# Kernel tuning notes

Measured on AMD Instinct MI355X. Metric: run time of the kernel, lower is better.

Reference implementation:

```python
import jax, jax.numpy as jnp
import numpy as np

N = 50000      # nodes
E = 600000     # edges (avg degree 12)
F_IN = 128     # num_features
H = 128        # hidden_feats (== F_IN so both conv layers share weight shapes)
C = 10         # num_classes
L = 2          # num_layers


def setup_inputs() -> dict:
    key = jax.random.key(0)
    ks = jax.random.split(key, 12)
    s = 0.05
    x = jax.random.normal(ks[0], (N, F_IN), dtype=jnp.float32)
    edge_index = jax.random.randint(ks[1], (2, E), 0, N, dtype=jnp.int64)
    # Stacked per-layer TransformerConv params (heads=1): query/key/value/skip linears.
    Wq = jax.random.normal(ks[2], (L, H, F_IN), dtype=jnp.float32) * s
    bq = jax.random.normal(ks[3], (L, H), dtype=jnp.float32) * s
    Wk = jax.random.normal(ks[4], (L, H, F_IN), dtype=jnp.float32) * s
    bk = jax.random.normal(ks[5], (L, H), dtype=jnp.float32) * s
    Wv = jax.random.normal(ks[6], (L, H, F_IN), dtype=jnp.float32) * s
    bv = jax.random.normal(ks[7], (L, H), dtype=jnp.float32) * s
    Ws = jax.random.normal(ks[8], (L, H, F_IN), dtype=jnp.float32) * s
    bs = jax.random.normal(ks[9], (L, H), dtype=jnp.float32) * s
    fc_W = jax.random.normal(ks[10], (C, H), dtype=jnp.float32) * s
    fc_b = jax.random.normal(ks[11], (C,), dtype=jnp.float32) * s
    return {"x": x, "edge_index": edge_index, "Wq": Wq, "bq": bq, "Wk": Wk,
            "bk": bk, "Wv": Wv, "bv": bv, "Ws": Ws, "bs": bs,
            "fc_W": fc_W, "fc_b": fc_b}


def _transformer_conv(h, src, dst, Wq, bq, Wk, bk, Wv, bv, Ws, bs):
    # PyG TransformerConv, heads=1, concat=True, root_weight=True, eval mode.
    d = Wq.shape[0]
    scale = 1.0 / np.sqrt(d).astype(np.float32)
    q = h @ Wq.T + bq          # [N, d]
    k = h @ Wk.T + bk          # [N, d]
    v = h @ Wv.T + bv          # [N, d]
    # per-edge attention score: <q_dst, k_src> / sqrt(d)
    scores = jnp.sum(q[dst] * k[src], axis=-1) * scale   # [E]
    # scatter-softmax over incoming edges of each destination node
    m = jax.ops.segment_max(scores, dst, num_segments=N)           # [N]
    e = jnp.exp(scores - m[dst])                                   # [E]
    denom = jax.ops.segment_sum(e, dst, num_segments=N)            # [N]
    alpha = e / denom[dst]                                         # [E]
    agg = jax.ops.segment_sum(alpha[:, None] * v[src], dst, num_segments=N)  # [N, d]
    return agg + (h @ Ws.T + bs)  # root/skip connection


def reference(x, edge_index, Wq, bq, Wk, bk, Wv, bv, Ws, bs, fc_W, fc_b):
    src = edge_index[0]
    dst = edge_index[1]
    h = x
    for l in range(L):  # fixed small layer loop
        h = _transformer_conv(h, src, dst, Wq[l], bq[l], Wk[l], bk[l],
                              Wv[l], bv[l], Ws[l], bs[l])
        h = jax.nn.relu(h)  # dropout is identity in eval mode
    logits = h @ fc_W.T + fc_b  # [N, C]
    return jax.nn.log_softmax(logits, axis=1)
```

## Files before the change

kernel.cpp:

```cpp
#include <hip/hip_runtime.h>
#include <math.h>

#define N_NODES 50000
#define N_EDGES 600000
#define DIM 128
#define NCLS 10
#define MTILES 391
#define CHUNKS_PER_TILE 2048
#define NB_SCAN 49

typedef _Float16 h2 __attribute__((ext_vector_type(2)));
typedef _Float16 half8 __attribute__((ext_vector_type(8)));
typedef __attribute__((ext_vector_type(4))) float f32x4;

__device__ inline h2 pkh(float a, float b) {
    auto r = __builtin_amdgcn_cvt_pkrtz(a, b);
    return *(h2*)&r;
}
__device__ inline unsigned h2u(h2 v) { return *(unsigned*)&v; }
__device__ inline h2 u2h(unsigned u) { return *(h2*)&u; }
__device__ inline int imin(int a, int b) { return a < b ? a : b; }

__device__ inline float dot2acc(h2 a, h2 b, float c) {
#if __has_builtin(__builtin_amdgcn_fdot2)
    return __builtin_amdgcn_fdot2(a, b, c, false);
#else
    return fmaf((float)a.x, (float)b.x, fmaf((float)a.y, (float)b.y, c));
#endif
}

__global__ void deg_kernel(const int* __restrict__ dst, int* __restrict__ deg) {
    int e = blockIdx.x * blockDim.x + threadIdx.x;
    if (e < N_EDGES) atomicAdd(&deg[dst[e]], 1);
}

__global__ __launch_bounds__(1024) void scan1_kernel(
        const int* __restrict__ deg, int* __restrict__ row_start,
        int* __restrict__ partials) {
    __shared__ int buf[1024];
    int b = blockIdx.x, t = threadIdx.x;
    int i = b * 1024 + t;
    buf[t] = (i < N_NODES) ? deg[i] : 0;
    __syncthreads();
    for (int off = 1; off < 1024; off <<= 1) {
        int tv = (t >= off) ? buf[t - off] : 0;
        __syncthreads();
        buf[t] += tv;
        __syncthreads();
    }
    if (i < N_NODES) row_start[i + 1] = buf[t];
    if (t == 1023) partials[b] = buf[1023];
}

__global__ __launch_bounds__(1024) void scan3_kernel(
        const int* __restrict__ partials, int* __restrict__ row_start,
        int* __restrict__ cursor) {
    __shared__ int boff_s;
    int b = blockIdx.x, t = threadIdx.x;
    if (t < 64) {
        int v = (t < b) ? partials[t] : 0;
        #pragma unroll
        for (int off = 32; off >= 1; off >>= 1) v += __shfl_xor(v, off);
        if (t == 0) boff_s = v;
    }
    __syncthreads();
    int boff = boff_s;
    int i = b * 1024 + t;
    if (i < N_NODES) {
        int val = row_start[i + 1] + boff;
        row_start[i + 1] = val;
        if (i + 1 < N_NODES) cursor[i + 1] = val;
    }
    if (i == 0) { row_start[0] = 0; cursor[0] = 0; }
}

__global__ void fill_kernel(const int* __restrict__ src, const int* __restrict__ dst,
                            int* __restrict__ cursor, int* __restrict__ col) {
    int e = blockIdx.x * blockDim.x + threadIdx.x;
    if (e < N_EDGES) {
        int pos = atomicAdd(&cursor[dst[e]], 1);
        col[pos] = src[e];
    }
}

__global__ __launch_bounds__(256) void convertw_kernel(
        const float* __restrict__ Wq, const float* __restrict__ Wk,
        const float* __restrict__ Wv, const float* __restrict__ Ws,
        unsigned short* __restrict__ wfrag) {
    int b = blockIdx.x;
    int l = b >> 2, m = b & 3;
    const float* W = (m == 0 ? Wq : m == 1 ? Wk : m == 2 ? Wv : Ws) + l * DIM * DIM;
    unsigned short* out = wfrag + (size_t)b * (CHUNKS_PER_TILE * 8);
    for (int i = threadIdx.x; i < CHUNKS_PER_TILE; i += 256) {
        int tile = i >> 6, lane = i & 63;
        int row = (tile >> 2) * 16 + (lane & 15);
        int k0 = (tile & 3) * 32 + (lane >> 4) * 8;
        const float4* p = (const float4*)(W + row * DIM + k0);
        float4 a = p[0], bb = p[1];
        uint4 o;
        o.x = h2u(pkh(a.x, a.y));  o.y = h2u(pkh(a.z, a.w));
        o.z = h2u(pkh(bb.x, bb.y)); o.w = h2u(pkh(bb.z, bb.w));
        *(uint4*)(out + (size_t)i * 8) = o;
    }
}

template <bool F32IN>
__global__ __launch_bounds__(512) void linear_kernel(
        const void* __restrict__ hb_,
        const unsigned short* __restrict__ wfrag,
        const float* __restrict__ bq, const float* __restrict__ bk,
        const float* __restrict__ bv, const float* __restrict__ bs,
        unsigned short* __restrict__ Qb, unsigned short* __restrict__ KVb,
        unsigned short* __restrict__ Sb) {
    __shared__ unsigned short hs[16384];
    __shared__ unsigned short wsm[16384];
    int tid = threadIdx.x;
    int tile = blockIdx.x;
    uint4* lh = (uint4*)hs;
    uint4* lw = (uint4*)wsm;
    #pragma unroll
    for (int j = 0; j < 4; ++j) {
        int i = tid + j * 512;
        int s = i >> 6, lane = i & 63;
        int row = tile * 128 + ((s >> 2) << 4) + (lane & 15);
        int k0 = ((s & 3) << 5) + ((lane >> 4) << 3);
        row = row < N_NODES ? row : N_NODES - 1;
        if (F32IN) {
            const float* hf = (const float*)hb_;
            const float4* p = (const float4*)(hf + (size_t)row * DIM + k0);
            float4 a = p[0], bb = p[1];
            uint4 o;
            o.x = h2u(pkh(a.x, a.y));  o.y = h2u(pkh(a.z, a.w));
            o.z = h2u(pkh(bb.x, bb.y)); o.w = h2u(pkh(bb.z, bb.w));
            lh[i] = o;
        } else {
            const unsigned short* hh = (const unsigned short*)hb_;
            lh[i] = *(const uint4*)(hh + (size_t)row * DIM + k0);
        }
    }
    int wave = tid >> 6, lane = tid & 63;
    int node = tile * 128 + wave * 16 + (lane & 15);
    int cq = (lane >> 4) * 4;

    #pragma unroll
    for (int m = 0; m < 4; ++m) {
        const uint4* gw = (const uint4*)(wfrag + (size_t)m * (CHUNKS_PER_TILE * 8));
        __syncthreads();
        #pragma unroll
        for (int j = 0; j < 4; ++j) lw[tid + j * 512] = gw[tid + j * 512];
        __syncthreads();

        f32x4 acc[8];
        #pragma unroll
        for (int nt = 0; nt < 8; ++nt) acc[nt] = (f32x4){0.f, 0.f, 0.f, 0.f};
        #pragma unroll
        for (int ks = 0; ks < 4; ++ks) {
            half8 hbv = *(const half8*)(lh + (wave * 4 + ks) * 64 + lane);
            #pragma unroll
            for (int nt = 0; nt < 8; ++nt)
                acc[nt] = __builtin_amdgcn_mfma_f32_16x16x32_f16(
                              *(const half8*)(lw + (nt * 4 + ks) * 64 + lane),
                              hbv, acc[nt], 0, 0, 0);
        }

        const float* bias = (m == 0 ? bq : m == 1 ? bk : m == 2 ? bv : bs);
        unsigned short* ob;
        unsigned ostr;
        if (m == 0)      { ob = Qb;        ostr = DIM; }
        else if (m == 1) { ob = KVb;       ostr = 256; }
        else if (m == 2) { ob = KVb + 128; ostr = 256; }
        else             { ob = Sb;        ostr = DIM; }
        if (node < N_NODES) {
            #pragma unroll
            for (int nt = 0; nt < 8; ++nt) {
                int colv = nt * 16 + cq;
                float4 bi = *(const float4*)(bias + colv);
                uint2 o;
                o.x = h2u(pkh(acc[nt][0] + bi.x, acc[nt][1] + bi.y));
                o.y = h2u(pkh(acc[nt][2] + bi.z, acc[nt][3] + bi.w));
                *(uint2*)(ob + (size_t)node * ostr + colv) = o;
            }
        }
    }
}

__global__ __launch_bounds__(256, 4) void attn_kernel(
        const unsigned short* __restrict__ Qb, const unsigned short* __restrict__ KVb,
        const unsigned short* __restrict__ Sb,
        const int* __restrict__ row_start, const int* __restrict__ col,
        unsigned short* __restrict__ hout) {
    int wave = threadIdx.x >> 6;
    int lane = threadIdx.x & 63;
    int g = lane >> 4, gl = lane & 15;
    int n = blockIdx.x * 4 + wave;
    if (n >= N_NODES) return;

    const char* KVc = (const char*)KVb + (gl << 4);
    const float qs = 0.08838834764831843f * 1.4426950408889634f;
    uint4 qu = *(const uint4*)((const char*)Qb + (((unsigned)n) << 8) + (gl << 4));
    h2 q0 = u2h(qu.x), q1 = u2h(qu.y), q2 = u2h(qu.z), q3 = u2h(qu.w);

    int e0 = row_start[n], e1 = row_start[n + 1];
    int deg = e1 - e0;
    const float NEG = -1.0e30f;
    float m = NEG, den = 0.f;
    h2 a0 = (h2)0, a1 = (h2)0, a2 = (h2)0, a3 = (h2)0;

#define LOAD4(eb_, k0_, v0_, k1_, v1_, k2_, v2_, k3_, v3_)                   \
    do {                                                                      \
        unsigned o0 = ((unsigned)col[imin((eb_), last)]) << 9;                \
        unsigned o1 = ((unsigned)col[imin((eb_) + 4, last)]) << 9;            \
        unsigned o2 = ((unsigned)col[imin((eb_) + 8, last)]) << 9;            \
        unsigned o3 = ((unsigned)col[imin((eb_) + 12, last)]) << 9;           \
        k0_ = *(const uint4*)(KVc + o0); v0_ = *(const uint4*)(KVc + o0 + 256); \
        k1_ = *(const uint4*)(KVc + o1); v1_ = *(const uint4*)(KVc + o1 + 256); \
        k2_ = *(const uint4*)(KVc + o2); v2_ = *(const uint4*)(KVc + o2 + 256); \
        k3_ = *(const uint4*)(KVc + o3); v3_ = *(const uint4*)(KVc + o3 + 256); \
    } while (0)

#define EDOT(kv) ({                                                           \
        float p_ = dot2acc(u2h((kv).x), q0, 0.f);                             \
        p_ = dot2acc(u2h((kv).y), q1, p_);                                    \
        p_ = dot2acc(u2h((kv).z), q2, p_);                                    \
        p_ = dot2acc(u2h((kv).w), q3, p_);                                    \
        p_ += __shfl_xor(p_, 1); p_ += __shfl_xor(p_, 2);                     \
        p_ += __shfl_xor(p_, 4); p_ += __shfl_xor(p_, 8);                     \
        p_; })

#define COMPUTE4(eb_, k0_, v0_, k1_, v1_, k2_, v2_, k3_, v3_)                 \
    do {                                                                      \
        float p0 = EDOT(k0_), p1 = EDOT(k1_), p2 = EDOT(k2_), p3 = EDOT(k3_); \
        p0 = (eb_) < e1      ? p0 * qs : NEG;                                 \
        p1 = (eb_) + 4 < e1  ? p1 * qs : NEG;                                 \
        p2 = (eb_) + 8 < e1  ? p2 * qs : NEG;                                 \
        p3 = (eb_) + 12 < e1 ? p3 * qs : NEG;                                 \
        float nm = fmaxf(m, fmaxf(fmaxf(p0, p1), fmaxf(p2, p3)));             \
        float fac = exp2f(m - nm);                                            \
        float w0 = exp2f(p0 - nm), w1 = exp2f(p1 - nm);                       \
        float w2 = exp2f(p2 - nm), w3 = exp2f(p3 - nm);                       \
        den = den * fac + (w0 + w1) + (w2 + w3);                              \
        h2 f2 = pkh(fac, fac);                                                \
        h2 w02 = pkh(w0, w0), w12 = pkh(w1, w1);                              \
        h2 w22 = pkh(w2, w2), w32 = pkh(w3, w3);                              \
        a0 = a0 * f2 + w02 * u2h(v0_.x) + w12 * u2h(v1_.x)                    \
                     + w22 * u2h(v2_.x) + w32 * u2h(v3_.x);                   \
        a1 = a1 * f2 + w02 * u2h(v0_.y) + w12 * u2h(v1_.y)                    \
                     + w22 * u2h(v2_.y) + w32 * u2h(v3_.y);                   \
        a2 = a2 * f2 + w02 * u2h(v0_.z) + w12 * u2h(v1_.z)                    \
                     + w22 * u2h(v2_.z) + w32 * u2h(v3_.z);                   \
        a3 = a3 * f2 + w02 * u2h(v0_.w) + w12 * u2h(v1_.w)                    \
                     + w22 * u2h(v2_.w) + w32 * u2h(v3_.w);                   \
        m = nm;                                                               \
    } while (0)

    if (deg > 0) {
        int last = e1 - 1;
        int B = (deg + 15) >> 4;
        int eb = e0 + g;
        uint4 k0, v0, k1, v1, k2, v2, k3, v3;
        LOAD4(eb, k0, v0, k1, v1, k2, v2, k3, v3);
        for (int b = 0;;) {
            uint4 nk0, nv0, nk1, nv1, nk2, nv2, nk3, nv3;
            bool more = (b + 1 < B);
            int ebn = eb + 16;
            if (more) LOAD4(ebn, nk0, nv0, nk1, nv1, nk2, nv2, nk3, nv3);
            COMPUTE4(eb, k0, v0, k1, v1, k2, v2, k3, v3);
            if (!more) break;
            eb = ebn; ++b;
            k0 = nk0; v0 = nv0; k1 = nk1; v1 = nv1;
            k2 = nk2; v2 = nv2; k3 = nk3; v3 = nv3;
        }
    }
#undef LOAD4
#undef EDOT
#undef COMPUTE4

    float acc[8];
    acc[0] = (float)a0.x; acc[1] = (float)a0.y;
    acc[2] = (float)a1.x; acc[3] = (float)a1.y;
    acc[4] = (float)a2.x; acc[5] = (float)a2.y;
    acc[6] = (float)a3.x; acc[7] = (float)a3.y;
    float M = m;
    M = fmaxf(M, __shfl_xor(M, 16));
    M = fmaxf(M, __shfl_xor(M, 32));
    float fac = exp2f(m - M);
    float d = den * fac;
    d += __shfl_xor(d, 16);
    d += __shfl_xor(d, 32);
    #pragma unroll
    for (int j = 0; j < 8; ++j) {
        float a = acc[j] * fac;
        a += __shfl_xor(a, 16);
        a += __shfl_xor(a, 32);
        acc[j] = a;
    }
    float inv = (d > 0.f) ? 1.f / d : 0.f;

    uint4 su = *(const uint4*)((const char*)Sb + (((unsigned)n) << 8) + (gl << 4));
    if (g == 0) {
        h2 s0 = u2h(su.x), s1 = u2h(su.y), s2 = u2h(su.z), s3 = u2h(su.w);
        uint4 o;
        o.x = h2u(pkh(fmaxf(fmaf(acc[0], inv, (float)s0.x), 0.f),
                      fmaxf(fmaf(acc[1], inv, (float)s0.y), 0.f)));
        o.y = h2u(pkh(fmaxf(fmaf(acc[2], inv, (float)s1.x), 0.f),
                      fmaxf(fmaf(acc[3], inv, (float)s1.y), 0.f)));
        o.z = h2u(pkh(fmaxf(fmaf(acc[4], inv, (float)s2.x), 0.f),
                      fmaxf(fmaf(acc[5], inv, (float)s2.y), 0.f)));
        o.w = h2u(pkh(fmaxf(fmaf(acc[6], inv, (float)s3.x), 0.f),
                      fmaxf(fmaf(acc[7], inv, (float)s3.y), 0.f)));
        *(uint4*)((char*)hout + (((unsigned)n) << 8) + (gl << 4)) = o;
    }
}

__global__ __launch_bounds__(256) void logits_kernel(
        const unsigned short* __restrict__ hb, const float* __restrict__ fcW,
        const float* __restrict__ fcb, float* __restrict__ out) {
    int wave = threadIdx.x >> 6, lane = threadIdx.x & 63;
    int n = blockIdx.x * 4 + wave;
    if (n >= N_NODES) return;
    unsigned hu = ((const unsigned*)hb)[(size_t)n * 64 + lane];
    h2 hh = u2h(hu);
    float hx = (float)hh.x, hy = (float)hh.y;
    float logit[NCLS];
    #pragma unroll
    for (int c = 0; c < NCLS; ++c) {
        float2 w = ((const float2*)(fcW + c * DIM))[lane];
        float p = hx * w.x + hy * w.y;
        #pragma unroll
        for (int off = 32; off >= 1; off >>= 1) p += __shfl_xor(p, off);
        logit[c] = p + fcb[c];
    }
    float mx = logit[0];
    #pragma unroll
    for (int c = 1; c < NCLS; ++c) mx = fmaxf(mx, logit[c]);
    float se = 0.f;
    #pragma unroll
    for (int c = 0; c < NCLS; ++c) se += __expf(logit[c] - mx);
    float lse = mx + logf(se);
    if (lane < NCLS) {
        float myv = 0.f;
        #pragma unroll
        for (int c = 0; c < NCLS; ++c) if (lane == c) myv = logit[c];
        out[(size_t)n * NCLS + lane] = myv - lse;
    }
}

extern "C" void kernel_launch(void* const* d_in, const int* in_sizes, int n_in,
                              void* d_out, int out_size, void* d_ws, size_t ws_size,
                              hipStream_t stream) {
    const float* x   = (const float*)d_in[0];
    const int*   ei  = (const int*)d_in[1];
    const float* Wq  = (const float*)d_in[2];
    const float* bq  = (const float*)d_in[3];
    const float* Wk  = (const float*)d_in[4];
    const float* bk  = (const float*)d_in[5];
    const float* Wv  = (const float*)d_in[6];
    const float* bv  = (const float*)d_in[7];
    const float* Ws  = (const float*)d_in[8];
    const float* bs  = (const float*)d_in[9];
    const float* fcW = (const float*)d_in[10];
    const float* fcb = (const float*)d_in[11];
    const int* src = ei;
    const int* dst = ei + N_EDGES;

    size_t NF = (size_t)N_NODES * DIM;
    unsigned short* Qb  = (unsigned short*)d_ws;
    unsigned short* Sb  = Qb + NF;
    unsigned short* KVb = Sb + NF;
    unsigned short* h1  = KVb + 2 * NF;
    unsigned short* wfrag = h1 + NF;
    int* ints      = (int*)(wfrag + 8 * CHUNKS_PER_TILE * 8);
    int* row_start = ints;
    int* cursor    = row_start + N_NODES + 1;
    int* col       = cursor + N_NODES;
    int* partials  = col + N_EDGES;

    (void)hipMemsetAsync(cursor, 0, N_NODES * sizeof(int), stream);
    deg_kernel<<<(N_EDGES + 255) / 256, 256, 0, stream>>>(dst, cursor);
    scan1_kernel<<<NB_SCAN, 1024, 0, stream>>>(cursor, row_start, partials);
    scan3_kernel<<<NB_SCAN, 1024, 0, stream>>>(partials, row_start, cursor);
    fill_kernel<<<(N_EDGES + 255) / 256, 256, 0, stream>>>(src, dst, cursor, col);

    convertw_kernel<<<8, 256, 0, stream>>>(Wq, Wk, Wv, Ws, wfrag);

    const int AGRID = (N_NODES + 3) / 4;

    linear_kernel<true><<<MTILES, 512, 0, stream>>>(x, wfrag, bq, bk, bv, bs,
                                                    Qb, KVb, Sb);
    attn_kernel<<<AGRID, 256, 0, stream>>>(Qb, KVb, Sb, row_start, col, h1);
    linear_kernel<false><<<MTILES, 512, 0, stream>>>(h1, wfrag + 4 * CHUNKS_PER_TILE * 8,
                                                     bq + DIM, bk + DIM, bv + DIM, bs + DIM,
                                                     Qb, KVb, Sb);
    attn_kernel<<<AGRID, 256, 0, stream>>>(Qb, KVb, Sb, row_start, col, h1);
    logits_kernel<<<AGRID, 256, 0, stream>>>(h1, fcW, fcb, (float*)d_out);
}
```

Measured before the change: 266.7 us.

## Store K/V in FP8 and fuse final logits into second attention kernel

The linear kernel now writes key and value projections as 8-bit floats instead of fp16, halving the bytes gathered per edge in the attention kernel. The attention kernel decodes FP8 into fp32 and accumulates in fp32 instead of packed fp16 math. The second attention pass is templated to compute the classifier logits and log-softmax directly, dropping the separate logits kernel and the h1 round trip. The lower K/V precision risks accuracy loss, and the extra decode and conversion instructions add ALU work.

```diff
diff --git a/kernel.cpp b/kernel.cpp
--- a/kernel.cpp
+++ b/kernel.cpp
@@ -12,6 +12,7 @@
 typedef _Float16 h2 __attribute__((ext_vector_type(2)));
 typedef _Float16 half8 __attribute__((ext_vector_type(8)));
 typedef __attribute__((ext_vector_type(4))) float f32x4;
+typedef unsigned char uchar;
 
 __device__ inline h2 pkh(float a, float b) {
     auto r = __builtin_amdgcn_cvt_pkrtz(a, b);
@@ -21,11 +22,45 @@
 __device__ inline h2 u2h(unsigned u) { return *(h2*)&u; }
 __device__ inline int imin(int a, int b) { return a < b ? a : b; }
 
-__device__ inline float dot2acc(h2 a, h2 b, float c) {
-#if __has_builtin(__builtin_amdgcn_fdot2)
-    return __builtin_amdgcn_fdot2(a, b, c, false);
+__device__ inline float dec1(unsigned b) {
+    unsigned s = b & 0x80, e = (b >> 3) & 15, m = b & 7;
+    float v = e ? ldexpf((float)(8 + m), (int)e - 10) : ldexpf((float)m, -9);
+    return s ? -v : v;
+}
+__device__ inline unsigned enc1(float f) {
+    float a = fabsf(f);
+    unsigned s = f < 0.f ? 0x80u : 0u;
+    if (!(a > 0.f)) return s;
+    if (a > 448.f) a = 448.f;
+    int e;
+    float mant = frexpf(a, &e);
+    if (e - 1 < -6) {
+        unsigned mq = (unsigned)rintf(ldexpf(a, 9));
+        return (mq >= 8) ? (s | 0x08u) : (s | mq);
+    }
+    unsigned mm = (unsigned)rintf(ldexpf(mant, 4));
+    unsigned E = (mm == 16) ? (unsigned)(e + 7) : (unsigned)(e + 6);
+    if (mm == 16) mm = 8;
+    return s | (E << 3) | (mm - 8);
+}
+__device__ inline void f8x4(unsigned u, float* o4) {
+#if __has_builtin(__builtin_amdgcn_cvt_pk_f32_fp8)
+    auto lo = __builtin_amdgcn_cvt_pk_f32_fp8(u, false);
+    auto hi = __builtin_amdgcn_cvt_pk_f32_fp8(u, true);
+    o4[0] = lo[0]; o4[1] = lo[1]; o4[2] = hi[0]; o4[3] = hi[1];
 #else
-    return fmaf((float)a.x, (float)b.x, fmaf((float)a.y, (float)b.y, c));
+    o4[0] = dec1(u & 255); o4[1] = dec1((u >> 8) & 255);
+    o4[2] = dec1((u >> 16) & 255); o4[3] = dec1(u >> 24);
+#endif
+}
+__device__ inline unsigned f8pk(float a, float b, float c, float d) {
+#if __has_builtin(__builtin_amdgcn_cvt_pk_fp8_f32)
+    int r = 0;
+    r = __builtin_amdgcn_cvt_pk_fp8_f32(a, b, r, false);
+    r = __builtin_amdgcn_cvt_pk_fp8_f32(c, d, r, true);
+    return (unsigned)r;
+#else
+    return enc1(a) | (enc1(b) << 8) | (enc1(c) << 16) | (enc1(d) << 24);
 #endif
 }
 
@@ -110,7 +145,7 @@
         const unsigned short* __restrict__ wfrag,
         const float* __restrict__ bq, const float* __restrict__ bk,
         const float* __restrict__ bv, const float* __restrict__ bs,
-        unsigned short* __restrict__ Qb, unsigned short* __restrict__ KVb,
+        unsigned short* __restrict__ Qb, uchar* __restrict__ KV8,
         unsigned short* __restrict__ Sb) {
     __shared__ unsigned short hs[16384];
     __shared__ unsigned short wsm[16384];
@@ -164,103 +199,125 @@
         }
 
         const float* bias = (m == 0 ? bq : m == 1 ? bk : m == 2 ? bv : bs);
-        unsigned short* ob;
-        unsigned ostr;
-        if (m == 0)      { ob = Qb;        ostr = DIM; }
-        else if (m == 1) { ob = KVb;       ostr = 256; }
-        else if (m == 2) { ob = KVb + 128; ostr = 256; }
-        else             { ob = Sb;        ostr = DIM; }
         if (node < N_NODES) {
-            #pragma unroll
-            for (int nt = 0; nt < 8; ++nt) {
-                int colv = nt * 16 + cq;
-                float4 bi = *(const float4*)(bias + colv);
-                uint2 o;
-                o.x = h2u(pkh(acc[nt][0] + bi.x, acc[nt][1] + bi.y));
-                o.y = h2u(pkh(acc[nt][2] + bi.z, acc[nt][3] + bi.w));
-                *(uint2*)(ob + (size_t)node * ostr + colv) = o;
+            if (m == 0 || m == 3) {
+                unsigned short* ob = (m == 0) ? Qb : Sb;
+                #pragma unroll
+                for (int nt = 0; nt < 8; ++nt) {
+                    int colv = nt * 16 + cq;
+                    float4 bi = *(const float4*)(bias + colv);
+                    uint2 o;
+                    o.x = h2u(pkh(acc[nt][0] + bi.x, acc[nt][1] + bi.y));
+                    o.y = h2u(pkh(acc[nt][2] + bi.z, acc[nt][3] + bi.w));
+                    *(uint2*)(ob + (size_t)node * DIM + colv) = o;
+                }
+            } else {
+                uchar* ob = KV8 + (size_t)node * 256 + (m == 1 ? 0 : 128);
+                #pragma unroll
+                for (int nt = 0; nt < 8; ++nt) {
+                    int colv = nt * 16 + cq;
+                    float4 bi = *(const float4*)(bias + colv);
+                    unsigned r = f8pk(acc[nt][0] + bi.x, acc[nt][1] + bi.y,
+                                      acc[nt][2] + bi.z, acc[nt][3] + bi.w);
+                    *(unsigned*)(ob + colv) = r;
+                }
             }
         }
     }
 }
 
+template <bool LOGITS>
 __global__ __launch_bounds__(256, 4) void attn_kernel(
-        const unsigned short* __restrict__ Qb, const unsigned short* __restrict__ KVb,
+        const unsigned short* __restrict__ Qb, const uchar* __restrict__ KV8,
         const unsigned short* __restrict__ Sb,
         const int* __restrict__ row_start, const int* __restrict__ col,
-        unsigned short* __restrict__ hout) {
+        unsigned short* __restrict__ hout, float* __restrict__ outF,
+        const float* __restrict__ fcW, const float* __restrict__ fcb) {
     int wave = threadIdx.x >> 6;
     int lane = threadIdx.x & 63;
     int g = lane >> 4, gl = lane & 15;
     int n = blockIdx.x * 4 + wave;
     if (n >= N_NODES) return;
 
-    const char* KVc = (const char*)KVb + (gl << 4);
+    const uchar* Kc = KV8 + (gl << 3);
+    const uchar* Vc = KV8 + 128 + (gl << 3);
     const float qs = 0.08838834764831843f * 1.4426950408889634f;
     uint4 qu = *(const uint4*)((const char*)Qb + (((unsigned)n) << 8) + (gl << 4));
-    h2 q0 = u2h(qu.x), q1 = u2h(qu.y), q2 = u2h(qu.z), q3 = u2h(qu.w);
+    h2 qh0 = u2h(qu.x), qh1 = u2h(qu.y), qh2 = u2h(qu.z), qh3 = u2h(qu.w);
+    float qf0 = (float)qh0.x * qs, qf1 = (float)qh0.y * qs;
+    float qf2 = (float)qh1.x * qs, qf3 = (float)qh1.y * qs;
+    float qf4 = (float)qh2.x * qs, qf5 = (float)qh2.y * qs;
+    float qf6 = (float)qh3.x * qs, qf7 = (float)qh3.y * qs;
 
     int e0 = row_start[n], e1 = row_start[n + 1];
     int deg = e1 - e0;
     const float NEG = -1.0e30f;
     float m = NEG, den = 0.f;
-    h2 a0 = (h2)0, a1 = (h2)0, a2 = (h2)0, a3 = (h2)0;
-
-#define LOAD4(eb_, k0_, v0_, k1_, v1_, k2_, v2_, k3_, v3_)                   \
-    do {                                                                      \
-        unsigned o0 = ((unsigned)col[imin((eb_), last)]) << 9;                \
-        unsigned o1 = ((unsigned)col[imin((eb_) + 4, last)]) << 9;            \
-        unsigned o2 = ((unsigned)col[imin((eb_) + 8, last)]) << 9;            \
-        unsigned o3 = ((unsigned)col[imin((eb_) + 12, last)]) << 9;           \
-        k0_ = *(const uint4*)(KVc + o0); v0_ = *(const uint4*)(KVc + o0 + 256); \
-        k1_ = *(const uint4*)(KVc + o1); v1_ = *(const uint4*)(KVc + o1 + 256); \
-        k2_ = *(const uint4*)(KVc + o2); v2_ = *(const uint4*)(KVc + o2 + 256); \
-        k3_ = *(const uint4*)(KVc + o3); v3_ = *(const uint4*)(KVc + o3 + 256); \
+    float acc[8];
+    #pragma unroll
+    for (int j = 0; j < 8; ++j) acc[j] = 0.f;
+
+#define LOAD4(eb_, k0_, v0_, k1_, v1_, k2_, v2_, k3_, v3_)                 \
+    do {                                                                    \
+        unsigned o0 = ((unsigned)col[imin((eb_), last)]) << 8;              \
+        unsigned o1 = ((unsigned)col[imin((eb_) + 4, last)]) << 8;          \
+        unsigned o2 = ((unsigned)col[imin((eb_) + 8, last)]) << 8;          \
+        unsigned o3 = ((unsigned)col[imin((eb_) + 12, last)]) << 8;         \
+        k0_ = *(const uint2*)(Kc + o0); v0_ = *(const uint2*)(Vc + o0);     \
+        k1_ = *(const uint2*)(Kc + o1); v1_ = *(const uint2*)(Vc + o1);     \
+        k2_ = *(const uint2*)(Kc + o2); v2_ = *(const uint2*)(Vc + o2);     \
+        k3_ = *(const uint2*)(Kc + o3); v3_ = *(const uint2*)(Vc + o3);     \
     } while (0)
 
-#define EDOT(kv) ({                                                           \
-        float p_ = dot2acc(u2h((kv).x), q0, 0.f);                             \
-        p_ = dot2acc(u2h((kv).y), q1, p_);                                    \
-        p_ = dot2acc(u2h((kv).z), q2, p_);                                    \
-        p_ = dot2acc(u2h((kv).w), q3, p_);                                    \
-        p_ += __shfl_xor(p_, 1); p_ += __shfl_xor(p_, 2);                     \
-        p_ += __shfl_xor(p_, 4); p_ += __shfl_xor(p_, 8);                     \
+#define EDOT8(ku_) ({                                                       \
+        float kk[8];                                                        \
+        f8x4((ku_).x, kk); f8x4((ku_).y, kk + 4);                           \
+        float p_ = qf0 * kk[0];                                             \
+        p_ = fmaf(qf1, kk[1], p_); p_ = fmaf(qf2, kk[2], p_);               \
+        p_ = fmaf(qf3, kk[3], p_); p_ = fmaf(qf4, kk[4], p_);               \
+        p_ = fmaf(qf5, kk[5], p_); p_ = fmaf(qf6, kk[6], p_);               \
+        p_ = fmaf(qf7, kk[7], p_);                                          \
+        p_ += __shfl_xor(p_, 1); p_ += __shfl_xor(p_, 2);                   \
+        p_ += __shfl_xor(p_, 4); p_ += __shfl_xor(p_, 8);                   \
         p_; })
 
-#define COMPUTE4(eb_, k0_, v0_, k1_, v1_, k2_, v2_, k3_, v3_)                 \
-    do {                                                                      \
-        float p0 = EDOT(k0_), p1 = EDOT(k1_), p2 = EDOT(k2_), p3 = EDOT(k3_); \
-        p0 = (eb_) < e1      ? p0 * qs : NEG;                                 \
-        p1 = (eb_) + 4 < e1  ? p1 * qs : NEG;                                 \
-        p2 = (eb_) + 8 < e1  ? p2 * qs : NEG;                                 \
-        p3 = (eb_) + 12 < e1 ? p3 * qs : NEG;                                 \
-        float nm = fmaxf(m, fmaxf(fmaxf(p0, p1), fmaxf(p2, p3)));             \
-        float fac = exp2f(m - nm);                                            \
-        float w0 = exp2f(p0 - nm), w1 = exp2f(p1 - nm);                       \
-        float w2 = exp2f(p2 - nm), w3 = exp2f(p3 - nm);                       \
-        den = den * fac + (w0 + w1) + (w2 + w3);                              \
-        h2 f2 = pkh(fac, fac);                                                \
-        h2 w02 = pkh(w0, w0), w12 = pkh(w1, w1);                              \
-        h2 w22 = pkh(w2, w2), w32 = pkh(w3, w3);                              \
-        a0 = a0 * f2 + w02 * u2h(v0_.x) + w12 * u2h(v1_.x)                    \
-                     + w22 * u2h(v2_.x) + w32 * u2h(v3_.x);                   \
-        a1 = a1 * f2 + w02 * u2h(v0_.y) + w12 * u2h(v1_.y)                    \
-                     + w22 * u2h(v2_.y) + w32 * u2h(v3_.y);                   \
-        a2 = a2 * f2 + w02 * u2h(v0_.z) + w12 * u2h(v1_.z)                    \
-                     + w22 * u2h(v2_.z) + w32 * u2h(v3_.z);                   \
-        a3 = a3 * f2 + w02 * u2h(v0_.w) + w12 * u2h(v1_.w)                    \
-                     + w22 * u2h(v2_.w) + w32 * u2h(v3_.w);                   \
-        m = nm;                                                               \
+#define ACCE(w_, vv_)                                                       \
+    do {                                                                    \
+        float tv[8];                                                        \
+        f8x4((vv_).x, tv); f8x4((vv_).y, tv + 4);                           \
+        acc[0] = fmaf(w_, tv[0], acc[0]); acc[1] = fmaf(w_, tv[1], acc[1]); \
+        acc[2] = fmaf(w_, tv[2], acc[2]); acc[3] = fmaf(w_, tv[3], acc[3]); \
+        acc[4] = fmaf(w_, tv[4], acc[4]); acc[5] = fmaf(w_, tv[5], acc[5]); \
+        acc[6] = fmaf(w_, tv[6], acc[6]); acc[7] = fmaf(w_, tv[7], acc[7]); \
+    } while (0)
+
+#define COMPUTE4(eb_, k0_, v0_, k1_, v1_, k2_, v2_, k3_, v3_)               \
+    do {                                                                    \
+        float p0 = EDOT8(k0_), p1 = EDOT8(k1_);                             \
+        float p2 = EDOT8(k2_), p3 = EDOT8(k3_);                             \
+        p0 = (eb_) < e1      ? p0 : NEG;                                    \
+        p1 = (eb_) + 4 < e1  ? p1 : NEG;                                    \
+        p2 = (eb_) + 8 < e1  ? p2 : NEG;                                    \
+        p3 = (eb_) + 12 < e1 ? p3 : NEG;                                    \
+        float nm = fmaxf(fmaxf(m, p0), fmaxf(fmaxf(p1, p2), p3));           \
+        float fac = exp2f(m - nm);                                          \
+        float w0 = exp2f(p0 - nm), w1 = exp2f(p1 - nm);                     \
+        float w2 = exp2f(p2 - nm), w3 = exp2f(p3 - nm);                     \
+        den = den * fac + (w0 + w1) + (w2 + w3);                            \
+        acc[0] *= fac; acc[1] *= fac; acc[2] *= fac; acc[3] *= fac;         \
+        acc[4] *= fac; acc[5] *= fac; acc[6] *= fac; acc[7] *= fac;         \
+        ACCE(w0, v0_); ACCE(w1, v1_); ACCE(w2, v2_); ACCE(w3, v3_);         \
+        m = nm;                                                             \
     } while (0)
 
     if (deg > 0) {
         int last = e1 - 1;
         int B = (deg + 15) >> 4;
         int eb = e0 + g;
-        uint4 k0, v0, k1, v1, k2, v2, k3, v3;
+        uint2 k0, v0, k1, v1, k2, v2, k3, v3;
         LOAD4(eb, k0, v0, k1, v1, k2, v2, k3, v3);
         for (int b = 0;;) {
-            uint4 nk0, nv0, nk1, nv1, nk2, nv2, nk3, nv3;
+            uint2 nk0, nv0, nk1, nv1, nk2, nv2, nk3, nv3;
             bool more = (b + 1 < B);
             int ebn = eb + 16;
             if (more) LOAD4(ebn, nk0, nv0, nk1, nv1, nk2, nv2, nk3, nv3);
@@ -272,24 +329,20 @@
         }
     }
 #undef LOAD4
-#undef EDOT
+#undef EDOT8
+#undef ACCE
 #undef COMPUTE4
 
-    float acc[8];
-    acc[0] = (float)a0.x; acc[1] = (float)a0.y;
-    acc[2] = (float)a1.x; acc[3] = (float)a1.y;
-    acc[4] = (float)a2.x; acc[5] = (float)a2.y;
-    acc[6] = (float)a3.x; acc[7] = (float)a3.y;
     float M = m;
     M = fmaxf(M, __shfl_xor(M, 16));
     M = fmaxf(M, __shfl_xor(M, 32));
-    float fac = exp2f(m - M);
-    float d = den * fac;
+    float fc_ = exp2f(m - M);
+    float d = den * fc_;
     d += __shfl_xor(d, 16);
     d += __shfl_xor(d, 32);
     #pragma unroll
     for (int j = 0; j < 8; ++j) {
-        float a = acc[j] * fac;
+        float a = acc[j] * fc_;
         a += __shfl_xor(a, 16);
         a += __shfl_xor(a, 32);
         acc[j] = a;
@@ -297,51 +350,48 @@
     float inv = (d > 0.f) ? 1.f / d : 0.f;
 
     uint4 su = *(const uint4*)((const char*)Sb + (((unsigned)n) << 8) + (gl << 4));
-    if (g == 0) {
-        h2 s0 = u2h(su.x), s1 = u2h(su.y), s2 = u2h(su.z), s3 = u2h(su.w);
-        uint4 o;
-        o.x = h2u(pkh(fmaxf(fmaf(acc[0], inv, (float)s0.x), 0.f),
-                      fmaxf(fmaf(acc[1], inv, (float)s0.y), 0.f)));
-        o.y = h2u(pkh(fmaxf(fmaf(acc[2], inv, (float)s1.x), 0.f),
-                      fmaxf(fmaf(acc[3], inv, (float)s1.y), 0.f)));
-        o.z = h2u(pkh(fmaxf(fmaf(acc[4], inv, (float)s2.x), 0.f),
-                      fmaxf(fmaf(acc[5], inv, (float)s2.y), 0.f)));
-        o.w = h2u(pkh(fmaxf(fmaf(acc[6], inv, (float)s3.x), 0.f),
-                      fmaxf(fmaf(acc[7], inv, (float)s3.y), 0.f)));
-        *(uint4*)((char*)hout + (((unsigned)n) << 8) + (gl << 4)) = o;
-    }
-}
-
-__global__ __launch_bounds__(256) void logits_kernel(
-        const unsigned short* __restrict__ hb, const float* __restrict__ fcW,
-        const float* __restrict__ fcb, float* __restrict__ out) {
-    int wave = threadIdx.x >> 6, lane = threadIdx.x & 63;
-    int n = blockIdx.x * 4 + wave;
-    if (n >= N_NODES) return;
-    unsigned hu = ((const unsigned*)hb)[(size_t)n * 64 + lane];
-    h2 hh = u2h(hu);
-    float hx = (float)hh.x, hy = (float)hh.y;
-    float logit[NCLS];
-    #pragma unroll
-    for (int c = 0; c < NCLS; ++c) {
-        float2 w = ((const float2*)(fcW + c * DIM))[lane];
-        float p = hx * w.x + hy * w.y;
-        #pragma unroll
-        for (int off = 32; off >= 1; off >>= 1) p += __shfl_xor(p, off);
-        logit[c] = p + fcb[c];
-    }
-    float mx = logit[0];
-    #pragma unroll
-    for (int c = 1; c < NCLS; ++c) mx = fmaxf(mx, logit[c]);
-    float se = 0.f;
-    #pragma unroll
-    for (int c = 0; c < NCLS; ++c) se += __expf(logit[c] - mx);
-    float lse = mx + logf(se);
-    if (lane < NCLS) {
-        float myv = 0.f;
-        #pragma unroll
-        for (int c = 0; c < NCLS; ++c) if (lane == c) myv = logit[c];
-        out[(size_t)n * NCLS + lane] = myv - lse;
+    h2 s0 = u2h(su.x), s1 = u2h(su.y), s2 = u2h(su.z), s3 = u2h(su.w);
+    float o0 = fmaxf(fmaf(acc[0], inv, (float)s0.x), 0.f);
+    float o1 = fmaxf(fmaf(acc[1], inv, (float)s0.y), 0.f);
+    float o2 = fmaxf(fmaf(acc[2], inv, (float)s1.x), 0.f);
+    float o3 = fmaxf(fmaf(acc[3], inv, (float)s1.y), 0.f);
+    float o4 = fmaxf(fmaf(acc[4], inv, (float)s2.x), 0.f);
+    float o5 = fmaxf(fmaf(acc[5], inv, (float)s2.y), 0.f);
+    float o6 = fmaxf(fmaf(acc[6], inv, (float)s3.x), 0.f);
+    float o7 = fmaxf(fmaf(acc[7], inv, (float)s3.y), 0.f);
+
+    if (!LOGITS) {
+        if (g == 0) {
+            uint4 o;
+            o.x = h2u(pkh(o0, o1)); o.y = h2u(pkh(o2, o3));
+            o.z = h2u(pkh(o4, o5)); o.w = h2u(pkh(o6, o7));
+            *(uint4*)((char*)hout + (((unsigned)n) << 8) + (gl << 4)) = o;
+        }
+    } else {
+        float lg[NCLS];
+        #pragma unroll
+        for (int c = 0; c < NCLS; ++c) {
+            const float4* fw = (const float4*)(fcW + c * DIM + gl * 8);
+            float4 wa = fw[0], wb = fw[1];
+            float pc = o0 * wa.x + o1 * wa.y + o2 * wa.z + o3 * wa.w
+                     + o4 * wb.x + o5 * wb.y + o6 * wb.z + o7 * wb.w;
+            pc += __shfl_xor(pc, 1); pc += __shfl_xor(pc, 2);
+            pc += __shfl_xor(pc, 4); pc += __shfl_xor(pc, 8);
+            lg[c] = pc + fcb[c];
+        }
+        float mx = lg[0];
+        #pragma unroll
+        for (int c = 1; c < NCLS; ++c) mx = fmaxf(mx, lg[c]);
+        float se = 0.f;
+        #pragma unroll
+        for (int c = 0; c < NCLS; ++c) se += __expf(lg[c] - mx);
+        float lse = mx + logf(se);
+        if (g == 0 && gl < NCLS) {
+            float myv = 0.f;
+            #pragma unroll
+            for (int c = 0; c < NCLS; ++c) if (gl == c) myv = lg[c];
+            outF[(size_t)n * NCLS + gl] = myv - lse;
+        }
     }
 }
 
@@ -366,8 +416,8 @@
     size_t NF = (size_t)N_NODES * DIM;
     unsigned short* Qb  = (unsigned short*)d_ws;
     unsigned short* Sb  = Qb + NF;
-    unsigned short* KVb = Sb + NF;
-    unsigned short* h1  = KVb + 2 * NF;
+    uchar* KV8 = (uchar*)(Sb + NF);
+    unsigned short* h1  = (unsigned short*)(KV8 + (size_t)N_NODES * 256);
     unsigned short* wfrag = h1 + NF;
     int* ints      = (int*)(wfrag + 8 * CHUNKS_PER_TILE * 8);
     int* row_start = ints;
@@ -386,11 +436,12 @@
     const int AGRID = (N_NODES + 3) / 4;
 
     linear_kernel<true><<<MTILES, 512, 0, stream>>>(x, wfrag, bq, bk, bv, bs,
-                                                    Qb, KVb, Sb);
-    attn_kernel<<<AGRID, 256, 0, stream>>>(Qb, KVb, Sb, row_start, col, h1);
+                                                    Qb, KV8, Sb);
+    attn_kernel<false><<<AGRID, 256, 0, stream>>>(Qb, KV8, Sb, row_start, col,
+                                                  h1, nullptr, nullptr, nullptr);
     linear_kernel<false><<<MTILES, 512, 0, stream>>>(h1, wfrag + 4 * CHUNKS_PER_TILE * 8,
                                                      bq + DIM, bk + DIM, bv + DIM, bs + DIM,
-                                                     Qb, KVb, Sb);
-    attn_kernel<<<AGRID, 256, 0, stream>>>(Qb, KVb, Sb, row_start, col, h1);
-    logits_kernel<<<AGRID, 256, 0, stream>>>(h1, fcW, fcb, (float*)d_out);
-}
+                                                     Qb, KV8, Sb);
+    attn_kernel<true><<<AGRID, 256, 0, stream>>>(Qb, KV8, Sb, row_start, col,
+                                                 nullptr, (float*)d_out, fcW, fcb);
+}
```

Result: faster. 233.4 us (-12.5%).
